# Kernel tuning notes

Measured on AMD Instinct MI355X. Metric: run time of the kernel, lower is better.

## Reference

```python
import jax, jax.numpy as jnp
import numpy as np

N_NODES = 100000
N_EDGES = 1600000
IN_CH = 48
OUT_CH = 64
K = 2


def setup_inputs() -> dict:
    key = jax.random.key(0)
    k1, k2, k3, k4 = jax.random.split(key, 4)
    x = jax.random.normal(k1, (N_NODES, IN_CH), dtype=jnp.float32)
    edge_index = jax.random.randint(k2, (2, N_EDGES), 0, N_NODES, dtype=jnp.int64)
    W = jax.random.normal(k3, (IN_CH, OUT_CH), dtype=jnp.float32) * (1.0 / np.sqrt(IN_CH))
    b = jax.random.normal(k4, (OUT_CH,), dtype=jnp.float32) * 0.01
    return {"x": x, "edge_index": edge_index, "W": W, "b": b}


def _propagate(x, row, col):
    n = x.shape[0]
    # degree of each node counted over col (destination) indices
    deg = jax.ops.segment_sum(jnp.ones_like(col, dtype=x.dtype), col, num_segments=n)
    deg_inv_sqrt = jnp.where(deg > 0, jax.lax.rsqrt(jnp.where(deg > 0, deg, 1.0)), 0.0)
    norm = deg_inv_sqrt[row] * deg_inv_sqrt[col]  # [E]
    # gather-scale-scatter: out[col] += x[row] * norm
    msgs = x[row] * norm[:, None]  # [E, d]
    return jax.ops.segment_sum(msgs, col, num_segments=n)


def reference(x, edge_index, W, b):
    row, col = edge_index[0], edge_index[1]
    h = x
    for _ in range(K):
        h = _propagate(h, row, col)
    return h @ W + b
```

## Files before the change

### kernel.cpp

```cpp
#include <hip/hip_runtime.h>
#include <hip/hip_bf16.h>
#include <hip/hip_fp16.h>


#define N_NODES 100000
#define N_EDGES 1600000
#define IN_CH 48
#define OUT_CH 64
#define NBUCKETS 392
#define CAP 4608
#define EPB 8192
#define NBLK_EDGE 196
#define NBLK_BKT 391

__global__ void init_kernel(int* __restrict__ bucketCursor, int* __restrict__ binTotal) {
    int t = threadIdx.x;
    if (t < NBUCKETS) bucketCursor[t] = t * CAP;
    if (t < 64) binTotal[t] = 0;
}

__global__ void bucket_scatter_kernel(const int* __restrict__ row, const int* __restrict__ col,
                                      int* __restrict__ bucketCursor, int* __restrict__ edge_packed) {
    __shared__ int lh[NBUCKETS];
    __shared__ int lofs[NBUCKETS];
    __shared__ int lbase[NBUCKETS];
    __shared__ int stage[EPB];
    __shared__ unsigned short sbkt[EPB];
    __shared__ int wsum[4];
    int tid = threadIdx.x;
    int base = blockIdx.x * EPB;
    for (int i = tid; i < NBUCKETS; i += 256) lh[i] = 0;
    __syncthreads();
    #pragma unroll 4
    for (int k = 0; k < 32; k++) {
        int e = base + k * 256 + tid;
        if (e < N_EDGES) atomicAdd(&lh[col[e] >> 8], 1);
    }
    __syncthreads();
    {
        int c0 = (tid < 196) ? lh[2 * tid] : 0;
        int c1 = (tid < 196) ? lh[2 * tid + 1] : 0;
        int s = c0 + c1;
        int incl = s;
        int lane = tid & 63, w = tid >> 6;
        #pragma unroll
        for (int o = 1; o < 64; o <<= 1) {
            int v = __shfl_up(incl, o, 64);
            if (lane >= o) incl += v;
        }
        if (lane == 63) wsum[w] = incl;
        __syncthreads();
        int wbase = 0;
        for (int k = 0; k < w; k++) wbase += wsum[k];
        int ex = wbase + incl - s;
        if (tid < 196) {
            lofs[2 * tid]     = ex;
            lofs[2 * tid + 1] = ex + c0;
        }
    }
    __syncthreads();
    for (int i = tid; i < NBUCKETS; i += 256) {
        int c = lh[i];
        if (c > 0) lbase[i] = atomicAdd(&bucketCursor[i], c);
        lh[i] = 0;
    }
    __syncthreads();
    #pragma unroll 4
    for (int k = 0; k < 32; k++) {
        int e = base + k * 256 + tid;
        if (e < N_EDGES) {
            int c = col[e];
            int bkt = c >> 8;
            int r = atomicAdd(&lh[bkt], 1);
            int slot = lofs[bkt] + r;
            stage[slot] = (row[e] << 8) | (c & 255);
            sbkt[slot] = (unsigned short)bkt;
        }
    }
    __syncthreads();
    int total = (base + EPB <= N_EDGES) ? EPB : (N_EDGES - base);
    for (int i = tid; i < total; i += 256) {
        int bkt = sbkt[i];
        int dst = lbase[bkt] + (i - lofs[bkt]);
        if (dst < (bkt + 1) * CAP)
            edge_packed[dst] = stage[i];
    }
}

__global__ void fine_sort_kernel(const int* __restrict__ edge_packed,
                                 const int* __restrict__ bucketCursor,
                                 const float* __restrict__ x,
                                 int* __restrict__ edge_src,
                                 int* __restrict__ deg, int* __restrict__ start,
                                 float* __restrict__ dis, int* __restrict__ binTotal,
                                 __half2* __restrict__ xs) {
    __shared__ int fh[256];
    __shared__ int cur[256];
    __shared__ int bh[64];
    __shared__ float fdis[256];
    __shared__ int wsum2[4];
    int b = blockIdx.x;
    int t = threadIdx.x;
    int s0 = b * CAP;
    int s1 = min(bucketCursor[b], (b + 1) * CAP);
    int nodeBase = b << 8;
    fh[t] = 0;
    if (t < 64) bh[t] = 0;
    __syncthreads();
    for (int j = s0 + t; j < s1; j += 256)
        atomicAdd(&fh[edge_packed[j] & 255], 1);
    __syncthreads();
    int c = fh[t];
    int incl = c;
    {
        int sl = t & 63, sw = t >> 6;
        #pragma unroll
        for (int o = 1; o < 64; o <<= 1) {
            int v = __shfl_up(incl, o, 64);
            if (sl >= o) incl += v;
        }
        if (sl == 63) wsum2[sw] = incl;
        __syncthreads();
        int wbase = 0;
        for (int k = 0; k < sw; k++) wbase += wsum2[k];
        incl += wbase;
    }
    int ex = incl - c;
    int node = nodeBase + t;
    bool valid = (node < N_NODES);
    int d = c;
    float dv = (valid && d > 0) ? rsqrtf((float)d) : 0.0f;
    cur[t] = ex;
    fdis[t] = dv;
    if (valid) {
        deg[node] = d;
        start[node] = s0 + ex;
        dis[node] = dv;
        atomicAdd(&bh[min(d, 63)], 1);
    }
    __syncthreads();
    for (int i = t; i < 256 * 24; i += 256) {
        int ln = i / 24;
        int nd = nodeBase + ln;
        if (nd < N_NODES) {
            int ci = i - ln * 24;
            float dd = fdis[ln];
            float2 v = ((const float2*)x)[nd * 24 + ci];
            xs[nd * 24 + ci] = __floats2half2_rn(v.x * dd, v.y * dd);
        }
    }
    for (int j = s0 + t; j < s1; j += 256) {
        int rc = edge_packed[j];
        int p = atomicAdd(&cur[rc & 255], 1);
        edge_src[s0 + p] = rc >> 8;
    }
    __syncthreads();
    if (t < 64 && bh[t]) atomicAdd(&binTotal[t], bh[t]);
}

__global__ void binscan_kernel(const int* __restrict__ binTotal, int* __restrict__ binCursor) {
    if (threadIdx.x == 0) {
        int s = 0;
        for (int k = 63; k >= 0; k--) { binCursor[k] = s; s += binTotal[k]; }
    }
}

__global__ void order_kernel(const int* __restrict__ deg, const int* __restrict__ start,
                             const float* __restrict__ dis, int* __restrict__ binCursor,
                             int4* __restrict__ nodeinfo, int n) {
    __shared__ int lhist[64];
    __shared__ int lbase[64];
    int i = blockIdx.x * 256 + threadIdx.x;
    if (threadIdx.x < 64) lhist[threadIdx.x] = 0;
    __syncthreads();
    int bin = 0, myrank = 0;
    if (i < n) {
        bin = min(deg[i], 63);
        myrank = atomicAdd(&lhist[bin], 1);
    }
    __syncthreads();
    if (threadIdx.x < 64 && lhist[threadIdx.x] > 0)
        lbase[threadIdx.x] = atomicAdd(&binCursor[threadIdx.x], lhist[threadIdx.x]);
    __syncthreads();
    if (i < n)
        nodeinfo[lbase[bin] + myrank] = make_int4(i, start[i], deg[i], __float_as_int(dis[i]));
}

#define LOAD3(p, v0, v1, v2) { v0 = (p)[0]; v1 = (p)[1]; v2 = (p)[2]; }
#define ACC6(v0, v1, v2) { \
    float2 u0 = __half22float2(v0), u1 = __half22float2(v1), u2 = __half22float2(v2); \
    a0 += u0.x; a1 += u0.y; a2 += u1.x; a3 += u1.y; a4 += u2.x; a5 += u2.y; }
#define ACC6B(v0, v1, v2) { \
    float2 u0 = __half22float2(v0), u1 = __half22float2(v1), u2 = __half22float2(v2); \
    b0 += u0.x; b1 += u0.y; b2 += u1.x; b3 += u1.y; b4 += u2.x; b5 += u2.y; }

#define DECLD(P) __half2 P##00,P##01,P##02,P##10,P##11,P##12,P##20,P##21,P##22,P##30,P##31,P##32
#define DECLS(S) int S##0, S##1, S##2, S##3
#define LOADSRC(S) { S##0 = edge_src[j]; S##1 = edge_src[j+1]; \
                     S##2 = edge_src[j+2]; S##3 = edge_src[j+3]; j += 4; }
#define ISSUED(P, S, basep) { \
    const __half2* q0 = basep + S##0 * 24 + lane3; \
    const __half2* q1 = basep + S##1 * 24 + lane3; \
    const __half2* q2 = basep + S##2 * 24 + lane3; \
    const __half2* q3 = basep + S##3 * 24 + lane3; \
    P##00 = q0[0]; P##01 = q0[1]; P##02 = q0[2]; \
    P##10 = q1[0]; P##11 = q1[1]; P##12 = q1[2]; \
    P##20 = q2[0]; P##21 = q2[1]; P##22 = q2[2]; \
    P##30 = q3[0]; P##31 = q3[1]; P##32 = q3[2]; }
#define CONSUMED(P) { ACC6(P##00,P##01,P##02); ACC6B(P##10,P##11,P##12); \
                      ACC6(P##20,P##21,P##22); ACC6B(P##30,P##31,P##32); }

#define GATHER_PIPELINE(basep) { \
    int m = (e - s) >> 2; \
    DECLD(A); DECLD(B); \
    DECLS(sa); DECLS(sb); \
    if (m >= 2) { \
        LOADSRC(sa); LOADSRC(sb); \
        ISSUED(A, sa, basep); \
        m -= 2; \
        while (m >= 2) { \
            LOADSRC(sa); \
            ISSUED(B, sb, basep); \
            CONSUMED(A); \
            LOADSRC(sb); \
            ISSUED(A, sa, basep); \
            CONSUMED(B); \
            m -= 2; \
        } \
        if (m == 1) { \
            LOADSRC(sa); \
            ISSUED(B, sb, basep); \
            CONSUMED(A); \
            ISSUED(A, sa, basep); \
            CONSUMED(B); \
            CONSUMED(A); \
        } else { \
            ISSUED(B, sb, basep); \
            CONSUMED(A); \
            CONSUMED(B); \
        } \
    } else if (m == 1) { \
        LOADSRC(sa); \
        ISSUED(A, sa, basep); \
        CONSUMED(A); \
    } \
    for (; j < e; ++j) { \
        const __half2* p0 = basep + edge_src[j] * 24 + lane3; \
        __half2 v00, v01, v02; \
        LOAD3(p0, v00, v01, v02); \
        ACC6(v00, v01, v02); \
    } \
    a0 += b0; a1 += b1; a2 += b2; a3 += b3; a4 += b4; a5 += b5; }

__global__ void gather1_kernel(const __half2* __restrict__ xs,
                               const int* __restrict__ edge_src,
                               const int4* __restrict__ nodeinfo,
                               __half2* __restrict__ h1) {
    int g = blockIdx.x * 32 + (threadIdx.x >> 3);
    int lane3 = (threadIdx.x & 7) * 3;
    int4 ni = nodeinfo[g];
    int node = ni.x, s = ni.y, e = s + ni.z;
    float dv = __int_as_float(ni.w);
    float a0 = 0, a1 = 0, a2 = 0, a3 = 0, a4 = 0, a5 = 0;
    float b0 = 0, b1 = 0, b2 = 0, b3 = 0, b4 = 0, b5 = 0;
    int j = s;
    GATHER_PIPELINE(xs);
    float sc = dv * dv;
    __half2* q = h1 + node * 24 + lane3;
    q[0] = __floats2half2_rn(a0 * sc, a1 * sc);
    q[1] = __floats2half2_rn(a2 * sc, a3 * sc);
    q[2] = __floats2half2_rn(a4 * sc, a5 * sc);
}

__global__ void gather2_gemm_kernel(const __half2* __restrict__ h1,
                                    const int* __restrict__ edge_src,
                                    const int4* __restrict__ nodeinfo,
                                    const float* __restrict__ W,
                                    const float* __restrict__ bias,
                                    float* __restrict__ out) {
    __shared__ float sW[IN_CH * OUT_CH];
    __shared__ float sb[OUT_CH];
    __shared__ float sh[32][IN_CH + 1];

    for (int i = threadIdx.x; i < IN_CH * OUT_CH; i += 256) sW[i] = W[i];
    if (threadIdx.x < OUT_CH) sb[threadIdx.x] = bias[threadIdx.x];

    int nl = threadIdx.x >> 3;
    int lane = threadIdx.x & 7;
    int lane3 = lane * 3;
    int g = blockIdx.x * 32 + nl;
    int4 ni = nodeinfo[g];
    int node = ni.x, s = ni.y, e = s + ni.z;
    float dv = __int_as_float(ni.w);

    float a0 = 0, a1 = 0, a2 = 0, a3 = 0, a4 = 0, a5 = 0;
    float b0 = 0, b1 = 0, b2 = 0, b3 = 0, b4 = 0, b5 = 0;
    int j = s;
    GATHER_PIPELINE(h1);
    int c0 = 6 * lane;
    sh[nl][c0 + 0] = a0 * dv;
    sh[nl][c0 + 1] = a1 * dv;
    sh[nl][c0 + 2] = a2 * dv;
    sh[nl][c0 + 3] = a3 * dv;
    sh[nl][c0 + 4] = a4 * dv;
    sh[nl][c0 + 5] = a5 * dv;
    __syncthreads();

    int j0 = lane * 8;
    float acc[8];
    #pragma unroll
    for (int i = 0; i < 8; i++) acc[i] = sb[j0 + i];
    for (int k = 0; k < IN_CH; k++) {
        float s0 = sh[nl][k];
        #pragma unroll
        for (int i = 0; i < 8; i++) acc[i] += s0 * sW[k * OUT_CH + j0 + i];
    }
    float4* o = (float4*)(out + (size_t)node * OUT_CH + j0);
    o[0] = make_float4(acc[0], acc[1], acc[2], acc[3]);
    o[1] = make_float4(acc[4], acc[5], acc[6], acc[7]);
}

extern "C" void kernel_launch(void* const* d_in, const int* in_sizes, int n_in,
                              void* d_out, int out_size, void* d_ws, size_t ws_size,
                              hipStream_t stream) {
    const float* x   = (const float*)d_in[0];
    const int*   ei  = (const int*)d_in[1];
    const float* W   = (const float*)d_in[2];
    const float* b   = (const float*)d_in[3];
    float* out = (float*)d_out;

    const int* row = ei;
    const int* col = ei + N_EDGES;

    int* ws_i = (int*)d_ws;
    int* bucketCursor = ws_i;
    int* binTotal     = ws_i + 512;
    int* binCursor    = ws_i + 576;
    int* deg          = ws_i + 1024;
    int* start        = ws_i + 101376;
    float* dis        = (float*)(ws_i + 201728);
    int4* nodeinfo    = (int4*)(ws_i + 302080);
    int* edge_packed  = ws_i + 703488;
    int* edge_src     = ws_i + 2509824;
    __half2* xs       = (__half2*)(ws_i + 4316160);
    __half2* h1       = (__half2*)(ws_i + 6716160);

    init_kernel<<<1, 512, 0, stream>>>(bucketCursor, binTotal);
    bucket_scatter_kernel<<<NBLK_EDGE, 256, 0, stream>>>(row, col, bucketCursor, edge_packed);
    fine_sort_kernel<<<NBLK_BKT, 256, 0, stream>>>(edge_packed, bucketCursor, x,
                                                   edge_src, deg, start, dis, binTotal, xs);
    binscan_kernel<<<1, 64, 0, stream>>>(binTotal, binCursor);
    order_kernel<<<(N_NODES + 255) / 256, 256, 0, stream>>>(deg, start, dis, binCursor,
                                                            nodeinfo, N_NODES);

    gather1_kernel<<<N_NODES / 32, 256, 0, stream>>>(xs, edge_src, nodeinfo, h1);
    gather2_gemm_kernel<<<N_NODES / 32, 256, 0, stream>>>(h1, edge_src, nodeinfo, W, b, out);
}
```

Before: 228.2 us.

## Widen gather pipeline to 8 edges, split scaling kernel, smaller scatter blocks

The gather pipeline now keeps 8 edges per stage in flight instead of 4, which raises memory-level parallelism at the cost of more registers. Launch bounds are added to the gather kernels to keep occupancy. Edges per bucket-scatter block drop from 8192 to 2048, giving 782 blocks, so the scatter spreads across more CUs. The x-scaling-to-half step moves out of fine_sort into its own fully parallel kernel, which adds one launch.

```diff
diff --git a/kernel.cpp b/kernel.cpp
--- a/kernel.cpp
+++ b/kernel.cpp
@@ -9,8 +9,9 @@
 #define OUT_CH 64
 #define NBUCKETS 392
 #define CAP 4608
-#define EPB 8192
-#define NBLK_EDGE 196
+#define EPB 2048
+#define EPR 8
+#define NBLK_EDGE 782
 #define NBLK_BKT 391
 
 __global__ void init_kernel(int* __restrict__ bucketCursor, int* __restrict__ binTotal) {
@@ -31,8 +32,8 @@
     int base = blockIdx.x * EPB;
     for (int i = tid; i < NBUCKETS; i += 256) lh[i] = 0;
     __syncthreads();
-    #pragma unroll 4
-    for (int k = 0; k < 32; k++) {
+    #pragma unroll
+    for (int k = 0; k < EPR; k++) {
         int e = base + k * 256 + tid;
         if (e < N_EDGES) atomicAdd(&lh[col[e] >> 8], 1);
     }
@@ -65,8 +66,8 @@
         lh[i] = 0;
     }
     __syncthreads();
-    #pragma unroll 4
-    for (int k = 0; k < 32; k++) {
+    #pragma unroll
+    for (int k = 0; k < EPR; k++) {
         int e = base + k * 256 + tid;
         if (e < N_EDGES) {
             int c = col[e];
@@ -89,15 +90,12 @@
 
 __global__ void fine_sort_kernel(const int* __restrict__ edge_packed,
                                  const int* __restrict__ bucketCursor,
-                                 const float* __restrict__ x,
                                  int* __restrict__ edge_src,
                                  int* __restrict__ deg, int* __restrict__ start,
-                                 float* __restrict__ dis, int* __restrict__ binTotal,
-                                 __half2* __restrict__ xs) {
+                                 float* __restrict__ dis, int* __restrict__ binTotal) {
     __shared__ int fh[256];
     __shared__ int cur[256];
     __shared__ int bh[64];
-    __shared__ float fdis[256];
     __shared__ int wsum2[4];
     int b = blockIdx.x;
     int t = threadIdx.x;
@@ -131,7 +129,6 @@
     int d = c;
     float dv = (valid && d > 0) ? rsqrtf((float)d) : 0.0f;
     cur[t] = ex;
-    fdis[t] = dv;
     if (valid) {
         deg[node] = d;
         start[node] = s0 + ex;
@@ -139,16 +136,6 @@
         atomicAdd(&bh[min(d, 63)], 1);
     }
     __syncthreads();
-    for (int i = t; i < 256 * 24; i += 256) {
-        int ln = i / 24;
-        int nd = nodeBase + ln;
-        if (nd < N_NODES) {
-            int ci = i - ln * 24;
-            float dd = fdis[ln];
-            float2 v = ((const float2*)x)[nd * 24 + ci];
-            xs[nd * 24 + ci] = __floats2half2_rn(v.x * dd, v.y * dd);
-        }
-    }
     for (int j = s0 + t; j < s1; j += 256) {
         int rc = edge_packed[j];
         int p = atomicAdd(&cur[rc & 255], 1);
@@ -156,6 +143,19 @@
     }
     __syncthreads();
     if (t < 64 && bh[t]) atomicAdd(&binTotal[t], bh[t]);
+}
+
+__global__ void scale_kernel(const float* __restrict__ x, const float* __restrict__ dis,
+                             __half2* __restrict__ xs) {
+    int g = blockIdx.x * 32 + (threadIdx.x >> 3);
+    int c = (threadIdx.x & 7) * 3;
+    float dd = dis[g];
+    const float2* px = (const float2*)x + g * 24 + c;
+    float2 v0 = px[0], v1 = px[1], v2 = px[2];
+    __half2* q = xs + g * 24 + c;
+    q[0] = __floats2half2_rn(v0.x * dd, v0.y * dd);
+    q[1] = __floats2half2_rn(v1.x * dd, v1.y * dd);
+    q[2] = __floats2half2_rn(v2.x * dd, v2.y * dd);
 }
 
 __global__ void binscan_kernel(const int* __restrict__ binTotal, int* __restrict__ binCursor) {
@@ -186,7 +186,6 @@
         nodeinfo[lbase[bin] + myrank] = make_int4(i, start[i], deg[i], __float_as_int(dis[i]));
 }
 
-#define LOAD3(p, v0, v1, v2) { v0 = (p)[0]; v1 = (p)[1]; v2 = (p)[2]; }
 #define ACC6(v0, v1, v2) { \
     float2 u0 = __half22float2(v0), u1 = __half22float2(v1), u2 = __half22float2(v2); \
     a0 += u0.x; a1 += u0.y; a2 += u1.x; a3 += u1.y; a4 += u2.x; a5 += u2.y; }
@@ -194,68 +193,75 @@
     float2 u0 = __half22float2(v0), u1 = __half22float2(v1), u2 = __half22float2(v2); \
     b0 += u0.x; b1 += u0.y; b2 += u1.x; b3 += u1.y; b4 += u2.x; b5 += u2.y; }
 
-#define DECLD(P) __half2 P##00,P##01,P##02,P##10,P##11,P##12,P##20,P##21,P##22,P##30,P##31,P##32
-#define DECLS(S) int S##0, S##1, S##2, S##3
-#define LOADSRC(S) { S##0 = edge_src[j]; S##1 = edge_src[j+1]; \
-                     S##2 = edge_src[j+2]; S##3 = edge_src[j+3]; j += 4; }
-#define ISSUED(P, S, basep) { \
-    const __half2* q0 = basep + S##0 * 24 + lane3; \
-    const __half2* q1 = basep + S##1 * 24 + lane3; \
-    const __half2* q2 = basep + S##2 * 24 + lane3; \
-    const __half2* q3 = basep + S##3 * 24 + lane3; \
-    P##00 = q0[0]; P##01 = q0[1]; P##02 = q0[2]; \
-    P##10 = q1[0]; P##11 = q1[1]; P##12 = q1[2]; \
-    P##20 = q2[0]; P##21 = q2[1]; P##22 = q2[2]; \
-    P##30 = q3[0]; P##31 = q3[1]; P##32 = q3[2]; }
-#define CONSUMED(P) { ACC6(P##00,P##01,P##02); ACC6B(P##10,P##11,P##12); \
-                      ACC6(P##20,P##21,P##22); ACC6B(P##30,P##31,P##32); }
-
-#define GATHER_PIPELINE(basep) { \
-    int m = (e - s) >> 2; \
-    DECLD(A); DECLD(B); \
-    DECLS(sa); DECLS(sb); \
+#define DECLD8(P) __half2 P##00,P##01,P##02,P##10,P##11,P##12,P##20,P##21,P##22, \
+                          P##30,P##31,P##32,P##40,P##41,P##42,P##50,P##51,P##52, \
+                          P##60,P##61,P##62,P##70,P##71,P##72
+#define DECLS8(S) int S##0,S##1,S##2,S##3,S##4,S##5,S##6,S##7
+#define LOADSRC8(S) { S##0 = edge_src[j];   S##1 = edge_src[j+1]; \
+                      S##2 = edge_src[j+2]; S##3 = edge_src[j+3]; \
+                      S##4 = edge_src[j+4]; S##5 = edge_src[j+5]; \
+                      S##6 = edge_src[j+6]; S##7 = edge_src[j+7]; j += 8; }
+#define ISSUE8(P, S, basep) { \
+    const __half2* q; \
+    q = basep + S##0 * 24 + lane3; P##00 = q[0]; P##01 = q[1]; P##02 = q[2]; \
+    q = basep + S##1 * 24 + lane3; P##10 = q[0]; P##11 = q[1]; P##12 = q[2]; \
+    q = basep + S##2 * 24 + lane3; P##20 = q[0]; P##21 = q[1]; P##22 = q[2]; \
+    q = basep + S##3 * 24 + lane3; P##30 = q[0]; P##31 = q[1]; P##32 = q[2]; \
+    q = basep + S##4 * 24 + lane3; P##40 = q[0]; P##41 = q[1]; P##42 = q[2]; \
+    q = basep + S##5 * 24 + lane3; P##50 = q[0]; P##51 = q[1]; P##52 = q[2]; \
+    q = basep + S##6 * 24 + lane3; P##60 = q[0]; P##61 = q[1]; P##62 = q[2]; \
+    q = basep + S##7 * 24 + lane3; P##70 = q[0]; P##71 = q[1]; P##72 = q[2]; }
+#define CONSUME8(P) { ACC6(P##00,P##01,P##02); ACC6B(P##10,P##11,P##12); \
+                      ACC6(P##20,P##21,P##22); ACC6B(P##30,P##31,P##32); \
+                      ACC6(P##40,P##41,P##42); ACC6B(P##50,P##51,P##52); \
+                      ACC6(P##60,P##61,P##62); ACC6B(P##70,P##71,P##72); }
+
+#define GATHER_PIPELINE8(basep) { \
+    int m = (e - s) >> 3; \
+    DECLD8(A); DECLD8(B); \
+    DECLS8(sa); DECLS8(sb); \
     if (m >= 2) { \
-        LOADSRC(sa); LOADSRC(sb); \
-        ISSUED(A, sa, basep); \
+        LOADSRC8(sa); LOADSRC8(sb); \
+        ISSUE8(A, sa, basep); \
         m -= 2; \
         while (m >= 2) { \
-            LOADSRC(sa); \
-            ISSUED(B, sb, basep); \
-            CONSUMED(A); \
-            LOADSRC(sb); \
-            ISSUED(A, sa, basep); \
-            CONSUMED(B); \
+            LOADSRC8(sa); \
+            ISSUE8(B, sb, basep); \
+            CONSUME8(A); \
+            LOADSRC8(sb); \
+            ISSUE8(A, sa, basep); \
+            CONSUME8(B); \
             m -= 2; \
         } \
         if (m == 1) { \
-            LOADSRC(sa); \
-            ISSUED(B, sb, basep); \
-            CONSUMED(A); \
-            ISSUED(A, sa, basep); \
-            CONSUMED(B); \
-            CONSUMED(A); \
+            LOADSRC8(sa); \
+            ISSUE8(B, sb, basep); \
+            CONSUME8(A); \
+            ISSUE8(A, sa, basep); \
+            CONSUME8(B); \
+            CONSUME8(A); \
         } else { \
-            ISSUED(B, sb, basep); \
-            CONSUMED(A); \
-            CONSUMED(B); \
+            ISSUE8(B, sb, basep); \
+            CONSUME8(A); \
+            CONSUME8(B); \
         } \
     } else if (m == 1) { \
-        LOADSRC(sa); \
-        ISSUED(A, sa, basep); \
-        CONSUMED(A); \
+        LOADSRC8(sa); \
+        ISSUE8(A, sa, basep); \
+        CONSUME8(A); \
     } \
     for (; j < e; ++j) { \
         const __half2* p0 = basep + edge_src[j] * 24 + lane3; \
-        __half2 v00, v01, v02; \
-        LOAD3(p0, v00, v01, v02); \
+        __half2 v00 = p0[0], v01 = p0[1], v02 = p0[2]; \
         ACC6(v00, v01, v02); \
     } \
     a0 += b0; a1 += b1; a2 += b2; a3 += b3; a4 += b4; a5 += b5; }
 
-__global__ void gather1_kernel(const __half2* __restrict__ xs,
-                               const int* __restrict__ edge_src,
-                               const int4* __restrict__ nodeinfo,
-                               __half2* __restrict__ h1) {
+__global__ void __launch_bounds__(256, 4)
+gather1_kernel(const __half2* __restrict__ xs,
+               const int* __restrict__ edge_src,
+               const int4* __restrict__ nodeinfo,
+               __half2* __restrict__ h1) {
     int g = blockIdx.x * 32 + (threadIdx.x >> 3);
     int lane3 = (threadIdx.x & 7) * 3;
     int4 ni = nodeinfo[g];
@@ -264,7 +270,7 @@
     float a0 = 0, a1 = 0, a2 = 0, a3 = 0, a4 = 0, a5 = 0;
     float b0 = 0, b1 = 0, b2 = 0, b3 = 0, b4 = 0, b5 = 0;
     int j = s;
-    GATHER_PIPELINE(xs);
+    GATHER_PIPELINE8(xs);
     float sc = dv * dv;
     __half2* q = h1 + node * 24 + lane3;
     q[0] = __floats2half2_rn(a0 * sc, a1 * sc);
@@ -272,12 +278,13 @@
     q[2] = __floats2half2_rn(a4 * sc, a5 * sc);
 }
 
-__global__ void gather2_gemm_kernel(const __half2* __restrict__ h1,
-                                    const int* __restrict__ edge_src,
-                                    const int4* __restrict__ nodeinfo,
-                                    const float* __restrict__ W,
-                                    const float* __restrict__ bias,
-                                    float* __restrict__ out) {
+__global__ void __launch_bounds__(256, 4)
+gather2_gemm_kernel(const __half2* __restrict__ h1,
+                    const int* __restrict__ edge_src,
+                    const int4* __restrict__ nodeinfo,
+                    const float* __restrict__ W,
+                    const float* __restrict__ bias,
+                    float* __restrict__ out) {
     __shared__ float sW[IN_CH * OUT_CH];
     __shared__ float sb[OUT_CH];
     __shared__ float sh[32][IN_CH + 1];
@@ -296,7 +303,7 @@
     float a0 = 0, a1 = 0, a2 = 0, a3 = 0, a4 = 0, a5 = 0;
     float b0 = 0, b1 = 0, b2 = 0, b3 = 0, b4 = 0, b5 = 0;
     int j = s;
-    GATHER_PIPELINE(h1);
+    GATHER_PIPELINE8(h1);
     int c0 = 6 * lane;
     sh[nl][c0 + 0] = a0 * dv;
     sh[nl][c0 + 1] = a1 * dv;
@@ -347,8 +354,9 @@
 
     init_kernel<<<1, 512, 0, stream>>>(bucketCursor, binTotal);
     bucket_scatter_kernel<<<NBLK_EDGE, 256, 0, stream>>>(row, col, bucketCursor, edge_packed);
-    fine_sort_kernel<<<NBLK_BKT, 256, 0, stream>>>(edge_packed, bucketCursor, x,
-                                                   edge_src, deg, start, dis, binTotal, xs);
+    fine_sort_kernel<<<NBLK_BKT, 256, 0, stream>>>(edge_packed, bucketCursor,
+                                                   edge_src, deg, start, dis, binTotal);
+    scale_kernel<<<N_NODES / 32, 256, 0, stream>>>(x, dis, xs);
     binscan_kernel<<<1, 64, 0, stream>>>(binTotal, binCursor);
     order_kernel<<<(N_NODES + 255) / 256, 256, 0, stream>>>(deg, start, dis, binCursor,
                                                             nodeinfo, N_NODES);
```

After: 229.3 us. Within noise of the previous version (+0.5%).
